# Optimization experiments

Hardware: AMD Instinct MI355X
Metric: run time of the kernel (lower is better)

The kernel has to match this reference:

```python
import jax, jax.numpy as jnp
import numpy as np

B, C, H, W = 16, 64, 256, 256


def setup_inputs() -> dict:
    key = jax.random.key(0)
    ks = jax.random.split(key, 4)
    scale = 1.0 / np.sqrt(C)
    return {
        "x": jax.random.normal(ks[0], (B, C, H, W), dtype=jnp.float32),
        "g_w": jax.random.normal(ks[1], (C, C), dtype=jnp.float32) * scale,
        "g_b": jnp.zeros((C,), dtype=jnp.float32),
        "theta_w": jax.random.normal(ks[2], (C, C), dtype=jnp.float32) * scale,
        "theta_b": jnp.zeros((C,), dtype=jnp.float32),
        "phi_w": jax.random.normal(ks[3], (C, C), dtype=jnp.float32) * scale,
        "phi_b": jnp.zeros((C,), dtype=jnp.float32),
    }


def reference(x, g_w, g_b, theta_w, theta_b, phi_w, phi_b):
    b, c, h, w = x.shape
    hw = h * w
    xf = x.reshape(b, c, hw)  # [B, C, HW]

    def proj(wt, bs):
        # 1x1 conv == channel-mixing linear: out[b,o,n] = sum_c wt[o,c] * x[b,c,n] + bs[o]
        return jnp.einsum('oc,bcn->bon', wt, xf) + bs[None, :, None]

    g_y = jax.nn.softmax(proj(g_w, g_b), axis=1)              # softmax over channels
    theta_x = jax.nn.softmax(proj(theta_w, theta_b), axis=-1)  # softmax over HW
    phi_x = proj(phi_w, phi_b)

    # similarity = phi_x @ theta_x^T  -> [B, C, C]
    similarity = jnp.einsum('bcn,bdn->bcd', phi_x, theta_x)
    # attention = similarity @ g_y   -> [B, C, HW]
    attention = jnp.einsum('bcd,bdn->bcn', similarity, g_y).reshape(b, c, h, w)

    return jax.nn.leaky_relu(x + attention, negative_slope=0.1)
```

## Files before the change

### kernel.cpp

```cpp
#include <hip/hip_runtime.h>
#include <hip/hip_fp16.h>
#include <cstdint>
#include <cstddef>

#define BATCH 16
#define CH 64
#define HWN 65536
#define NBLK 64
#define PAD 72
#define ACHUNK 8

typedef __attribute__((ext_vector_type(8))) _Float16 half8;
typedef __attribute__((ext_vector_type(4))) float f32x4;

static const size_t SP_OFF = 0;
static const size_t ZP_OFF = SP_OFF + (size_t)BATCH * NBLK * 4096 * 4;
static const size_t M_OFF  = ZP_OFF + (size_t)BATCH * NBLK * 4 * 64 * 4;

__device__ __forceinline__ half8 load_frag_f32(const float* p) {
    const float4 w0 = *(const float4*)p;
    const float4 w1 = *(const float4*)(p + 4);
    half8 f;
    f[0] = (_Float16)w0.x; f[1] = (_Float16)w0.y;
    f[2] = (_Float16)w0.z; f[3] = (_Float16)w0.w;
    f[4] = (_Float16)w1.x; f[5] = (_Float16)w1.y;
    f[6] = (_Float16)w1.z; f[7] = (_Float16)w1.w;
    return f;
}

__global__ __launch_bounds__(256) void proj_s(
    const float* __restrict__ x,
    const float* __restrict__ thw, const float* __restrict__ thb,
    const float* __restrict__ phw, const float* __restrict__ phb,
    float* __restrict__ Sp, float* __restrict__ Zp)
{
    __shared__ __align__(16) ushort xt[64 * PAD];
    __shared__ __align__(16) ushort El[64 * PAD];
    __shared__ __align__(16) ushort Pl[64 * PAD];
    const int b   = blockIdx.y;
    const int blk = blockIdx.x;
    const int tid = threadIdx.x;
    const int wid = tid >> 6;
    const int l   = tid & 63;
    const int lr  = l & 15;
    const int lg  = l >> 4;

    half8 Wf[2][4][2];
#pragma unroll
    for (int p = 0; p < 2; p++) {
        const float* wsrc = p ? phw : thw;
#pragma unroll
        for (int ot = 0; ot < 4; ot++)
#pragma unroll
            for (int g = 0; g < 2; g++)
                Wf[p][ot][g] = load_frag_f32(wsrc + (ot * 16 + lr) * 64 + g * 32 + lg * 8);
    }
    float bT[16], bP[16];
#pragma unroll
    for (int ot = 0; ot < 4; ot++)
#pragma unroll
        for (int i = 0; i < 4; i++) {
            bT[ot * 4 + i] = thb[ot * 16 + lg * 4 + i];
            bP[ot * 4 + i] = phb[ot * 16 + lg * 4 + i];
        }

    f32x4 Sacc[4];
#pragma unroll
    for (int j = 0; j < 4; j++) Sacc[j] = (f32x4){0.f, 0.f, 0.f, 0.f};
    float z[16];
#pragma unroll
    for (int k = 0; k < 16; k++) z[k] = 0.f;

    const float* xb = x + (size_t)b * CH * HWN;
    const int sch = tid >> 4;
    const int spx = (tid & 15) * 4;

    for (int chk = 0; chk < 16; chk++) {
        const int nb = blk * 1024 + chk * 64;

#pragma unroll
        for (int it = 0; it < 4; it++) {
            const int ch = sch + it * 16;
            const float4 v = *(const float4*)(xb + (size_t)ch * HWN + nb + spx);
            xt[(spx + 0) * PAD + ch] = __half_as_ushort(__float2half(v.x));
            xt[(spx + 1) * PAD + ch] = __half_as_ushort(__float2half(v.y));
            xt[(spx + 2) * PAD + ch] = __half_as_ushort(__float2half(v.z));
            xt[(spx + 3) * PAD + ch] = __half_as_ushort(__float2half(v.w));
        }
        __syncthreads();

        const int ncol = wid * 16 + lr;
        half8 xf0 = *(const half8*)(xt + ncol * PAD + lg * 8);
        half8 xf1 = *(const half8*)(xt + ncol * PAD + 32 + lg * 8);
#pragma unroll
        for (int ot = 0; ot < 4; ot++) {
            const int off = (ot * 16 + lg * 4) * PAD + ncol;
            f32x4 acc = {bT[ot * 4 + 0], bT[ot * 4 + 1], bT[ot * 4 + 2], bT[ot * 4 + 3]};
            acc = __builtin_amdgcn_mfma_f32_16x16x32_f16(Wf[0][ot][0], xf0, acc, 0, 0, 0);
            acc = __builtin_amdgcn_mfma_f32_16x16x32_f16(Wf[0][ot][1], xf1, acc, 0, 0, 0);
#pragma unroll
            for (int i = 0; i < 4; i++) {
                float e = __expf(acc[i]);
                z[ot * 4 + i] += e;
                El[off + i * PAD] = __half_as_ushort(__float2half(e));
            }
            f32x4 pcc = {bP[ot * 4 + 0], bP[ot * 4 + 1], bP[ot * 4 + 2], bP[ot * 4 + 3]};
            pcc = __builtin_amdgcn_mfma_f32_16x16x32_f16(Wf[1][ot][0], xf0, pcc, 0, 0, 0);
            pcc = __builtin_amdgcn_mfma_f32_16x16x32_f16(Wf[1][ot][1], xf1, pcc, 0, 0, 0);
#pragma unroll
            for (int i = 0; i < 4; i++)
                Pl[off + i * PAD] = __half_as_ushort(__float2half(pcc[i]));
        }
        __syncthreads();

        const ushort* arow = Pl + (wid * 16 + lr) * PAD;
#pragma unroll
        for (int g = 0; g < 2; g++) {
            const int coff = g * 32 + lg * 8;
            half8 af = *(const half8*)(arow + coff);
#pragma unroll
            for (int j = 0; j < 4; j++) {
                half8 bf = *(const half8*)(El + (j * 16 + lr) * PAD + coff);
                Sacc[j] = __builtin_amdgcn_mfma_f32_16x16x32_f16(af, bf, Sacc[j], 0, 0, 0);
            }
        }
    }

    float* sp = Sp + (size_t)(b * NBLK + blk) * 4096;
#pragma unroll
    for (int j = 0; j < 4; j++)
#pragma unroll
        for (int i = 0; i < 4; i++)
            sp[(wid * 16 + lg * 4 + i) * 64 + j * 16 + lr] = Sacc[j][i];

#pragma unroll
    for (int k = 0; k < 16; k++) {
        float v = z[k];
        v += __shfl_xor(v, 1, 64);
        v += __shfl_xor(v, 2, 64);
        v += __shfl_xor(v, 4, 64);
        v += __shfl_xor(v, 8, 64);
        z[k] = v;
    }
    if (lr == 0) {
        float* zp = Zp + ((size_t)(b * NBLK + blk) * 4 + wid) * 64;
#pragma unroll
        for (int t = 0; t < 4; t++)
#pragma unroll
            for (int i = 0; i < 4; i++)
                zp[t * 16 + lg * 4 + i] = z[t * 4 + i];
    }
}

__global__ __launch_bounds__(256) void normalize_S(
    const float* __restrict__ Sp, const float* __restrict__ Zp,
    float* __restrict__ M)
{
    const int b   = blockIdx.y;
    const int sl  = blockIdx.x;
    const int tid = threadIdx.x;
    __shared__ float Zl[64];
    if (tid < 64) {
        float s = 0.f;
        const float* zp = Zp + (size_t)b * (NBLK * 4) * 64 + tid;
        for (int k = 0; k < NBLK * 4; k++) s += zp[(size_t)k * 64];
        Zl[tid] = 1.0f / s;
    }
    __syncthreads();
    const float* sp = Sp + (size_t)b * NBLK * 4096;
    float* mp = M + (size_t)b * 4096;
#pragma unroll
    for (int h = 0; h < 2; h++) {
        const int idx = sl * 512 + h * 256 + tid;
        float s = 0.f;
        for (int k = 0; k < NBLK; k++) s += sp[(size_t)k * 4096 + idx];
        mp[idx] = s * Zl[idx & 63];
    }
}

__global__ __launch_bounds__(256) void attn_mfma(
    const float* __restrict__ x,
    const float* __restrict__ gw, const float* __restrict__ gb,
    const float* __restrict__ M,
    float* __restrict__ out)
{
    __shared__ __align__(16) ushort xt[128 * PAD];
    __shared__ __align__(16) ushort El[128 * PAD];
    const int b   = blockIdx.y;
    const int tid = threadIdx.x;
    const int wid = tid >> 6;
    const int l   = tid & 63;
    const int lr  = l & 15;
    const int lg  = l >> 4;

    const float* xb = x + (size_t)b * CH * HWN;
    float* outb = out + (size_t)b * CH * HWN;

    half8 Gf[4][2];
#pragma unroll
    for (int ot = 0; ot < 4; ot++)
#pragma unroll
        for (int kg = 0; kg < 2; kg++)
            Gf[ot][kg] = load_frag_f32(gw + (ot * 16 + lr) * 64 + kg * 32 + lg * 8);
    float bG[16];
#pragma unroll
    for (int ot = 0; ot < 4; ot++)
#pragma unroll
        for (int i = 0; i < 4; i++) bG[ot * 4 + i] = gb[ot * 16 + lg * 4 + i];

    half8 Mf[4][2];
    const float* Mb = M + (size_t)b * 4096;
#pragma unroll
    for (int ct = 0; ct < 4; ct++)
#pragma unroll
        for (int kg = 0; kg < 2; kg++)
            Mf[ct][kg] = load_frag_f32(Mb + (ct * 16 + lr) * 64 + kg * 32 + lg * 8);

    const int sch = tid >> 5;
    const int spx = (tid & 31) * 4;

    for (int chk = 0; chk < ACHUNK; chk++) {
        const int nb = blockIdx.x * (128 * ACHUNK) + chk * 128;

#pragma unroll
        for (int it = 0; it < 8; it++) {
            const int ch = sch + it * 8;
            const float4 v = *(const float4*)(xb + (size_t)ch * HWN + nb + spx);
            xt[(spx + 0) * PAD + ch] = __half_as_ushort(__float2half(v.x));
            xt[(spx + 1) * PAD + ch] = __half_as_ushort(__float2half(v.y));
            xt[(spx + 2) * PAD + ch] = __half_as_ushort(__float2half(v.z));
            xt[(spx + 3) * PAD + ch] = __half_as_ushort(__float2half(v.w));
        }
        __syncthreads();

        float rz[2];
#pragma unroll
        for (int nt = 0; nt < 2; nt++) {
            const int ncol = wid * 32 + nt * 16 + lr;
            half8 xf0 = *(const half8*)(xt + ncol * PAD + lg * 8);
            half8 xf1 = *(const half8*)(xt + ncol * PAD + 32 + lg * 8);

            float gy[4][4];
#pragma unroll
            for (int ot = 0; ot < 4; ot++) {
                f32x4 acc = {bG[ot * 4 + 0], bG[ot * 4 + 1], bG[ot * 4 + 2], bG[ot * 4 + 3]};
                acc = __builtin_amdgcn_mfma_f32_16x16x32_f16(Gf[ot][0], xf0, acc, 0, 0, 0);
                acc = __builtin_amdgcn_mfma_f32_16x16x32_f16(Gf[ot][1], xf1, acc, 0, 0, 0);
#pragma unroll
                for (int i = 0; i < 4; i++) gy[ot][i] = acc[i];
            }
            float m = gy[0][0];
#pragma unroll
            for (int ot = 0; ot < 4; ot++)
#pragma unroll
                for (int i = 0; i < 4; i++) m = fmaxf(m, gy[ot][i]);
            m = fmaxf(m, __shfl_xor(m, 16, 64));
            m = fmaxf(m, __shfl_xor(m, 32, 64));

            float zs = 0.f;
            ushort* erow = El + ncol * PAD;
#pragma unroll
            for (int ot = 0; ot < 4; ot++) {
                float e0 = __expf(gy[ot][0] - m);
                float e1 = __expf(gy[ot][1] - m);
                float e2 = __expf(gy[ot][2] - m);
                float e3 = __expf(gy[ot][3] - m);
                zs += e0 + e1 + e2 + e3;
                uint2 pk;
                pk.x = (uint)__half_as_ushort(__float2half(e0)) |
                       ((uint)__half_as_ushort(__float2half(e1)) << 16);
                pk.y = (uint)__half_as_ushort(__float2half(e2)) |
                       ((uint)__half_as_ushort(__float2half(e3)) << 16);
                *(uint2*)(erow + ot * 16 + lg * 4) = pk;
            }
            zs += __shfl_xor(zs, 16, 64);
            zs += __shfl_xor(zs, 32, 64);
            rz[nt] = 1.0f / zs;
        }

#pragma unroll
        for (int nt = 0; nt < 2; nt++) {
            const int ncol = wid * 32 + nt * 16 + lr;
            const ushort* brow = El + ncol * PAD;
            half8 bf0 = *(const half8*)(brow + lg * 8);
            half8 bf1 = *(const half8*)(brow + 32 + lg * 8);
            const float sc = rz[nt];
#pragma unroll
            for (int ct = 0; ct < 4; ct++) {
                f32x4 acc = {0.f, 0.f, 0.f, 0.f};
                acc = __builtin_amdgcn_mfma_f32_16x16x32_f16(Mf[ct][0], bf0, acc, 0, 0, 0);
                acc = __builtin_amdgcn_mfma_f32_16x16x32_f16(Mf[ct][1], bf1, acc, 0, 0, 0);
#pragma unroll
                for (int i = 0; i < 4; i++) {
                    const size_t off = (size_t)(ct * 16 + lg * 4 + i) * HWN + nb + ncol;
                    float v = xb[off] + acc[i] * sc;
                    outb[off] = (v >= 0.f) ? v : 0.1f * v;
                }
            }
        }
        __syncthreads();
    }
}

extern "C" void kernel_launch(void* const* d_in, const int* in_sizes, int n_in,
                              void* d_out, int out_size, void* d_ws, size_t ws_size,
                              hipStream_t stream)
{
    const float* x   = (const float*)d_in[0];
    const float* gw  = (const float*)d_in[1];
    const float* gb  = (const float*)d_in[2];
    const float* thw = (const float*)d_in[3];
    const float* thb = (const float*)d_in[4];
    const float* phw = (const float*)d_in[5];
    const float* phb = (const float*)d_in[6];
    float* out = (float*)d_out;

    char* ws = (char*)d_ws;
    float* Sp = (float*)(ws + SP_OFF);
    float* Zp = (float*)(ws + ZP_OFF);
    float* M  = (float*)(ws + M_OFF);

    dim3 blk(256);
    proj_s<<<dim3(NBLK, BATCH), blk, 0, stream>>>(x, thw, thb, phw, phb, Sp, Zp);
    normalize_S<<<dim3(8, BATCH), blk, 0, stream>>>(Sp, Zp, M);
    attn_mfma<<<dim3(HWN / (128 * ACHUNK), BATCH), blk, 0, stream>>>(x, gw, gb, M, out);
}
```

Before: 262.8 us.

## Swizzle transposed x tile in LDS, pack stores, and prefetch next chunk

Each thread now loads four channels of one pixel, packs them as fp16 and writes one 8-byte store into the LDS transpose tile, replacing four scalar 2-byte stores. The column offset is XOR-swizzled to cut bank conflicts on both the writes and the MFMA fragment reads. In proj_s the next chunk's global loads are issued right after the barrier, so they overlap with the MFMA work. The trade-off is scalar (non-vector) global loads and more registers held across the loop.

```diff
diff --git a/kernel.cpp b/kernel.cpp
--- a/kernel.cpp
+++ b/kernel.cpp
@@ -27,6 +27,12 @@
     f[6] = (_Float16)w1.z; f[7] = (_Float16)w1.w;
     return f;
 }
+
+__device__ __forceinline__ uint pack2h(float a, float b) {
+    return (uint)__half_as_ushort(__float2half(a)) |
+           ((uint)__half_as_ushort(__float2half(b)) << 16);
+}
+
 
 __global__ __launch_bounds__(256) void proj_s(
     const float* __restrict__ x,
@@ -72,26 +78,43 @@
     for (int k = 0; k < 16; k++) z[k] = 0.f;
 
     const float* xb = x + (size_t)b * CH * HWN;
-    const int sch = tid >> 4;
-    const int spx = (tid & 15) * 4;
+    const int spx = tid & 63;
+    const int chb = (tid >> 6) * 4;
+    const int ssw = ((spx >> 3) & 7) << 3;
+    ushort* xrow = xt + spx * PAD;
+
+    float xr[4][4];
+#pragma unroll
+    for (int it = 0; it < 4; it++)
+#pragma unroll
+        for (int c = 0; c < 4; c++)
+            xr[it][c] = xb[(size_t)(chb + 16 * it + c) * HWN + blk * 1024 + spx];
 
     for (int chk = 0; chk < 16; chk++) {
         const int nb = blk * 1024 + chk * 64;
 
 #pragma unroll
         for (int it = 0; it < 4; it++) {
-            const int ch = sch + it * 16;
-            const float4 v = *(const float4*)(xb + (size_t)ch * HWN + nb + spx);
-            xt[(spx + 0) * PAD + ch] = __half_as_ushort(__float2half(v.x));
-            xt[(spx + 1) * PAD + ch] = __half_as_ushort(__float2half(v.y));
-            xt[(spx + 2) * PAD + ch] = __half_as_ushort(__float2half(v.z));
-            xt[(spx + 3) * PAD + ch] = __half_as_ushort(__float2half(v.w));
+            uint2 pk;
+            pk.x = pack2h(xr[it][0], xr[it][1]);
+            pk.y = pack2h(xr[it][2], xr[it][3]);
+            *(uint2*)(xrow + ((chb + 16 * it) ^ ssw)) = pk;
         }
         __syncthreads();
 
+        if (chk + 1 < 16) {
+            const int nb2 = nb + 64;
+#pragma unroll
+            for (int it = 0; it < 4; it++)
+#pragma unroll
+                for (int c = 0; c < 4; c++)
+                    xr[it][c] = xb[(size_t)(chb + 16 * it + c) * HWN + nb2 + spx];
+        }
+
         const int ncol = wid * 16 + lr;
-        half8 xf0 = *(const half8*)(xt + ncol * PAD + lg * 8);
-        half8 xf1 = *(const half8*)(xt + ncol * PAD + 32 + lg * 8);
+        const int rsw  = ((ncol >> 3) & 7) << 3;
+        half8 xf0 = *(const half8*)(xt + ncol * PAD + ((lg * 8) ^ rsw));
+        half8 xf1 = *(const half8*)(xt + ncol * PAD + ((32 + lg * 8) ^ rsw));
 #pragma unroll
         for (int ot = 0; ot < 4; ot++) {
             const int off = (ot * 16 + lg * 4) * PAD + ncol;
@@ -216,20 +239,30 @@
         for (int kg = 0; kg < 2; kg++)
             Mf[ct][kg] = load_frag_f32(Mb + (ct * 16 + lr) * 64 + kg * 32 + lg * 8);
 
-    const int sch = tid >> 5;
-    const int spx = (tid & 31) * 4;
+    const int spx0 = tid & 63;
+    const int chb  = (tid >> 6) * 4;
 
     for (int chk = 0; chk < ACHUNK; chk++) {
         const int nb = blockIdx.x * (128 * ACHUNK) + chk * 128;
 
 #pragma unroll
-        for (int it = 0; it < 8; it++) {
-            const int ch = sch + it * 8;
-            const float4 v = *(const float4*)(xb + (size_t)ch * HWN + nb + spx);
-            xt[(spx + 0) * PAD + ch] = __half_as_ushort(__float2half(v.x));
-            xt[(spx + 1) * PAD + ch] = __half_as_ushort(__float2half(v.y));
-            xt[(spx + 2) * PAD + ch] = __half_as_ushort(__float2half(v.z));
-            xt[(spx + 3) * PAD + ch] = __half_as_ushort(__float2half(v.w));
+        for (int h = 0; h < 2; h++) {
+            const int spx = spx0 + 64 * h;
+            const int ssw = ((spx >> 3) & 7) << 3;
+            float v[4][4];
+#pragma unroll
+            for (int it = 0; it < 4; it++)
+#pragma unroll
+                for (int c = 0; c < 4; c++)
+                    v[it][c] = xb[(size_t)(chb + 16 * it + c) * HWN + nb + spx];
+            ushort* xrow = xt + spx * PAD;
+#pragma unroll
+            for (int it = 0; it < 4; it++) {
+                uint2 pk;
+                pk.x = pack2h(v[it][0], v[it][1]);
+                pk.y = pack2h(v[it][2], v[it][3]);
+                *(uint2*)(xrow + ((chb + 16 * it) ^ ssw)) = pk;
+            }
         }
         __syncthreads();
 
@@ -237,8 +270,9 @@
 #pragma unroll
         for (int nt = 0; nt < 2; nt++) {
             const int ncol = wid * 32 + nt * 16 + lr;
-            half8 xf0 = *(const half8*)(xt + ncol * PAD + lg * 8);
-            half8 xf1 = *(const half8*)(xt + ncol * PAD + 32 + lg * 8);
+            const int rsw  = ((ncol >> 3) & 7) << 3;
+            half8 xf0 = *(const half8*)(xt + ncol * PAD + ((lg * 8) ^ rsw));
+            half8 xf1 = *(const half8*)(xt + ncol * PAD + ((32 + lg * 8) ^ rsw));
 
             float gy[4][4];
 #pragma unroll
@@ -267,10 +301,8 @@
                 float e3 = __expf(gy[ot][3] - m);
                 zs += e0 + e1 + e2 + e3;
                 uint2 pk;
-                pk.x = (uint)__half_as_ushort(__float2half(e0)) |
-                       ((uint)__half_as_ushort(__float2half(e1)) << 16);
-                pk.y = (uint)__half_as_ushort(__float2half(e2)) |
-                       ((uint)__half_as_ushort(__float2half(e3)) << 16);
+                pk.x = pack2h(e0, e1);
+                pk.y = pack2h(e2, e3);
                 *(uint2*)(erow + ot * 16 + lg * 4) = pk;
             }
             zs += __shfl_xor(zs, 16, 64);
```

New measurement: 247.8 us. 5.7% less time.
